# Kernel optimization log

Measured on AMD Instinct MI355X. Metric: run time of the kernel, lower is better.

Reference implementation:

```python
import jax, jax.numpy as jnp
import numpy as np

LAMBDA_GEO = 0.5


def setup_inputs() -> dict:
    key = jax.random.key(0)
    embeddings = jax.random.normal(key, (4, 2048, 512), dtype=jnp.float32)
    return {"embeddings": embeddings}


def _geometric_loss(embeddings):
    b, s, d = embeddings.shape
    x = embeddings.reshape(b * s, d)  # [N, d]
    sq_norm = jnp.sum(x * x, axis=-1)  # [N]
    sq = sq_norm[:, None] + sq_norm[None, :] - 2.0 * (x @ x.T)  # [N, N]
    sq = jnp.maximum(sq, 0.0)
    dist = jnp.sqrt(sq)  # torch.cdist(p=2)
    return jnp.mean(jnp.exp(-dist * 0.1)) * 0.1


def reference(embeddings):
    geometric_loss = _geometric_loss(embeddings)
    total_geometric = LAMBDA_GEO * geometric_loss
    return geometric_loss, total_geometric
```

## Files before the change

kernel.cpp:

```cpp
#include <hip/hip_runtime.h>

#define NROWS 8192
#define DIM   512
#define NT    64
#define NTRI  (NT * (NT + 1) / 2)
#define NACC  64

typedef __attribute__((ext_vector_type(16))) float f32x16;
typedef __attribute__((ext_vector_type(8)))  int   i32x8;

__device__ __forceinline__ unsigned char f2e4m3(float x) {
    unsigned ux = __float_as_uint(x);
    unsigned s  = (ux >> 24) & 0x80u;
    float a = __uint_as_float(ux & 0x7FFFFFFFu);
    a = fminf(a, 448.0f);
    unsigned ua = __float_as_uint(a);
    int eb = (int)(ua >> 23);
    if (eb < 121) eb = 121;
    float step  = __uint_as_float((unsigned)(eb - 3) << 23);
    float istep = __uint_as_float((unsigned)(257 - eb) << 23);
    float q = rintf(a * istep) * step;
    q = fminf(q, 448.0f);
    if (q < 0.001953125f)
        return (unsigned char)s;
    unsigned uq = __float_as_uint(q);
    int eq = (int)(uq >> 23) - 127;
    unsigned byte;
    if (eq < -6) byte = (unsigned)(q * 512.0f);
    else         byte = (unsigned)((eq + 7) << 3) | ((uq >> 20) & 7u);
    return (unsigned char)(s | byte);
}

__global__ __launch_bounds__(256) void norm_convert_kernel(
    const float* __restrict__ X, unsigned char* __restrict__ Xq,
    float* __restrict__ norms, float* __restrict__ acc)
{
    const int tid  = threadIdx.x;
    const int lane = tid & 63;
    const int w    = tid >> 6;
    const int row  = blockIdx.x * 4 + w;

    if (blockIdx.x == 0 && tid < NACC) acc[tid] = 0.0f;

    const float* xr = X + (size_t)row * DIM + lane * 8;
    float4 v0 = *(const float4*)xr;
    float4 v1 = *(const float4*)(xr + 4);

    float s = 0.0f;
    s = fmaf(v0.x, v0.x, s); s = fmaf(v0.y, v0.y, s);
    s = fmaf(v0.z, v0.z, s); s = fmaf(v0.w, v0.w, s);
    s = fmaf(v1.x, v1.x, s); s = fmaf(v1.y, v1.y, s);
    s = fmaf(v1.z, v1.z, s); s = fmaf(v1.w, v1.w, s);

    union { unsigned char b[8]; uint2 v; } pk;
    pk.b[0] = f2e4m3(v0.x); pk.b[1] = f2e4m3(v0.y);
    pk.b[2] = f2e4m3(v0.z); pk.b[3] = f2e4m3(v0.w);
    pk.b[4] = f2e4m3(v1.x); pk.b[5] = f2e4m3(v1.y);
    pk.b[6] = f2e4m3(v1.z); pk.b[7] = f2e4m3(v1.w);

    const int slab = lane >> 3;
    const int cpos = (lane & 7) ^ (row & 7);
    *(uint2*)(Xq + (size_t)row * DIM + slab * 64 + cpos * 8) = pk.v;

    #pragma unroll
    for (int off = 32; off > 0; off >>= 1) s += __shfl_down(s, off, 64);
    if (lane == 0) norms[row] = s;
}

__device__ __forceinline__ void gload16(const void* g, void* l) {
    __builtin_amdgcn_global_load_lds(
        (const __attribute__((address_space(1))) unsigned int*)g,
        (__attribute__((address_space(3))) unsigned int*)l, 16, 0, 0);
}

__global__ __launch_bounds__(256, 4) void pair_loss_gemm_kernel(
    const unsigned char* __restrict__ Xq, const float* __restrict__ norms,
    float* __restrict__ acc)
{
    __shared__ __align__(16) char As0[8192];
    __shared__ __align__(16) char As1[8192];
    __shared__ __align__(16) char Bs0[8192];
    __shared__ __align__(16) char Bs1[8192];
    __shared__ float wsum[4];

    int t = blockIdx.x, bi = 0;
    while (t >= (NT - bi)) { t -= (NT - bi); bi++; }
    const int bj = bi + t;

    const int tid  = threadIdx.x;
    const int lane = tid & 63;
    const int w    = tid >> 6;

    const int rowA = bi * 128;
    const int rowB = bj * 128;

    f32x16 accv[2][2];
    #pragma unroll
    for (int a = 0; a < 2; a++)
        #pragma unroll
        for (int b = 0; b < 2; b++)
            #pragma unroll
            for (int r = 0; r < 16; r++) accv[a][b][r] = 0.0f;

    const int rs = w * 32 + (lane >> 2);
    const int cs = (lane & 3) * 16;
    const unsigned char* sA0 = Xq + (size_t)(rowA + rs) * DIM + cs;
    const unsigned char* sA1 = sA0 + (size_t)16 * DIM;
    const unsigned char* sB0 = Xq + (size_t)(rowB + rs) * DIM + cs;
    const unsigned char* sB1 = sB0 + (size_t)16 * DIM;
    const int ldw = w * 2048;

    const int rl = lane & 31;
    const int qh = lane >> 5;
    const int sw = lane & 7;
    const int wr = (w & 1) * 64;
    const int wc = (w >> 1) * 64;
    const int raoff = (wr + rl) * 64;
    const int rboff = (wc + rl) * 64;

    gload16(sA0, As0 + ldw);
    gload16(sA1, As0 + ldw + 1024);
    gload16(sB0, Bs0 + ldw);
    gload16(sB1, Bs0 + ldw + 1024);
    __syncthreads();

    char* curA = As0; char* nxtA = As1;
    char* curB = Bs0; char* nxtB = Bs1;

    #pragma unroll 1
    for (int k = 0; k < 8; k++) {
        const bool more = (k < 7);
        if (more) {
            const int ko = (k + 1) * 64;
            gload16(sA0 + ko, nxtA + ldw);
            gload16(sA1 + ko, nxtA + ldw + 1024);
            gload16(sB0 + ko, nxtB + ldw);
            gload16(sB1 + ko, nxtB + ldw + 1024);
        }

        union { long l[4]; i32x8 v; } fa0, fa1, fb0, fb1;
        #pragma unroll
        for (int i = 0; i < 4; i++) {
            const int fo = ((4 * qh + i) ^ sw) * 8;
            fa0.l[i] = *(const long*)(curA + raoff + fo);
            fa1.l[i] = *(const long*)(curA + raoff + 2048 + fo);
            fb0.l[i] = *(const long*)(curB + rboff + fo);
            fb1.l[i] = *(const long*)(curB + rboff + 2048 + fo);
        }

        accv[0][0] = __builtin_amdgcn_mfma_scale_f32_32x32x64_f8f6f4(
            fa0.v, fb0.v, accv[0][0], 0, 0, 0, 0x7F7F7F7F, 0, 0x7F7F7F7F);
        accv[0][1] = __builtin_amdgcn_mfma_scale_f32_32x32x64_f8f6f4(
            fa0.v, fb1.v, accv[0][1], 0, 0, 0, 0x7F7F7F7F, 0, 0x7F7F7F7F);
        accv[1][0] = __builtin_amdgcn_mfma_scale_f32_32x32x64_f8f6f4(
            fa1.v, fb0.v, accv[1][0], 0, 0, 0, 0x7F7F7F7F, 0, 0x7F7F7F7F);
        accv[1][1] = __builtin_amdgcn_mfma_scale_f32_32x32x64_f8f6f4(
            fa1.v, fb1.v, accv[1][1], 0, 0, 0, 0x7F7F7F7F, 0, 0x7F7F7F7F);

        if (more) {
            __syncthreads();
            char* tA = curA; curA = nxtA; nxtA = tA;
            char* tB = curB; curB = nxtB; nxtB = tB;
        }
    }

    const float wgt = (bi == bj) ? 1.0f : 2.0f;
    const int cl = lane & 31;
    const int rh = (lane >> 5) * 4;
    float lsum = 0.0f;
    #pragma unroll
    for (int a = 0; a < 2; a++) {
        const int gia = rowA + wr + a * 32;
        float ni[16];
        #pragma unroll
        for (int r = 0; r < 16; r++)
            ni[r] = norms[gia + (r & 3) + 8 * (r >> 2) + rh];
        #pragma unroll
        for (int b = 0; b < 2; b++) {
            const int gj = rowB + wc + b * 32 + cl;
            const float nj = norms[gj];
            #pragma unroll
            for (int r = 0; r < 16; r++) {
                const int gi = gia + (r & 3) + 8 * (r >> 2) + rh;
                float sq = fmaf(-2.0f, accv[a][b][r], ni[r] + nj);
                sq = fmaxf(sq, 0.0f);
                float term = __expf(-0.1f * sqrtf(sq));
                if (gi == gj) term = 1.0f;
                lsum += term;
            }
        }
    }
    lsum *= wgt;
    #pragma unroll
    for (int off = 32; off > 0; off >>= 1) lsum += __shfl_down(lsum, off, 64);
    if (lane == 0) wsum[w] = lsum;
    __syncthreads();
    if (tid == 0)
        atomicAdd(&acc[blockIdx.x & (NACC - 1)],
                  wsum[0] + wsum[1] + wsum[2] + wsum[3]);
}

__global__ void finalize_kernel(const float* __restrict__ acc,
                                float* __restrict__ out)
{
    const int lane = threadIdx.x;
    float s = (lane < NACC) ? acc[lane] : 0.0f;
    #pragma unroll
    for (int off = 32; off > 0; off >>= 1) s += __shfl_down(s, off, 64);
    if (lane == 0) {
        const float inv = 1.0f / ((float)NROWS * (float)NROWS);
        float loss = s * inv * 0.1f;
        out[0] = loss;
        out[1] = 0.5f * loss;
    }
}

extern "C" void kernel_launch(void* const* d_in, const int* in_sizes, int n_in,
                              void* d_out, int out_size, void* d_ws, size_t ws_size,
                              hipStream_t stream)
{
    const float* X = (const float*)d_in[0];
    float* out = (float*)d_out;

    char* ws = (char*)d_ws;
    float*         acc   = (float*)ws;
    float*         norms = (float*)(ws + 1024);
    unsigned char* Xq    = (unsigned char*)(ws + 1024 + 32768);

    norm_convert_kernel<<<NROWS / 4, 256, 0, stream>>>(X, Xq, norms, acc);
    pair_loss_gemm_kernel<<<NTRI, 256, 0, stream>>>(Xq, norms, acc);
    finalize_kernel<<<1, 64, 0, stream>>>(acc, out);
}
```

Before: 106.3 us.

## Double K-step per stage, 16-byte swizzled LDS reads, fuse finalize via last-block counter

The GEMM stage now loads 128 bytes of K per step (two 64-wide slabs), halving loop iterations and barriers. The fp8 swizzle changes from 8-byte to 16-byte granularity so fragments are read with uint4 LDS loads. setprio is raised around the MFMA block. The separate finalize kernel is replaced by a last-block atomic counter that reduces the accumulators in-kernel, saving a launch. LDS doubles to 64KB per block and occupancy hint drops from 4 to 2 blocks per CU.

```diff
diff --git a/kernel.cpp b/kernel.cpp
--- a/kernel.cpp
+++ b/kernel.cpp
@@ -40,7 +40,7 @@
     const int w    = tid >> 6;
     const int row  = blockIdx.x * 4 + w;
 
-    if (blockIdx.x == 0 && tid < NACC) acc[tid] = 0.0f;
+    if (blockIdx.x == 0 && tid < NACC + 1) acc[tid] = 0.0f;
 
     const float* xr = X + (size_t)row * DIM + lane * 8;
     float4 v0 = *(const float4*)xr;
@@ -59,8 +59,10 @@
     pk.b[6] = f2e4m3(v1.z); pk.b[7] = f2e4m3(v1.w);
 
     const int slab = lane >> 3;
-    const int cpos = (lane & 7) ^ (row & 7);
-    *(uint2*)(Xq + (size_t)row * DIM + slab * 64 + cpos * 8) = pk.v;
+    const int c16  = (lane >> 1) & 3;
+    const int cpos = c16 ^ ((row >> 1) & 3);
+    *(uint2*)(Xq + (size_t)row * DIM + slab * 64 + cpos * 16 + (lane & 1) * 8)
+        = pk.v;
 
     #pragma unroll
     for (int off = 32; off > 0; off >>= 1) s += __shfl_down(s, off, 64);
@@ -73,15 +75,16 @@
         (__attribute__((address_space(3))) unsigned int*)l, 16, 0, 0);
 }
 
-__global__ __launch_bounds__(256, 4) void pair_loss_gemm_kernel(
+__global__ __launch_bounds__(256, 2) void pair_loss_gemm_kernel(
     const unsigned char* __restrict__ Xq, const float* __restrict__ norms,
-    float* __restrict__ acc)
+    float* __restrict__ acc, float* __restrict__ out)
 {
-    __shared__ __align__(16) char As0[8192];
-    __shared__ __align__(16) char As1[8192];
-    __shared__ __align__(16) char Bs0[8192];
-    __shared__ __align__(16) char Bs1[8192];
+    __shared__ __align__(16) char As0[16384];
+    __shared__ __align__(16) char As1[16384];
+    __shared__ __align__(16) char Bs0[16384];
+    __shared__ __align__(16) char Bs1[16384];
     __shared__ float wsum[4];
+    __shared__ int lastflag;
 
     int t = blockIdx.x, bi = 0;
     while (t >= (NT - bi)) { t -= (NT - bi); bi++; }
@@ -102,60 +105,72 @@
             #pragma unroll
             for (int r = 0; r < 16; r++) accv[a][b][r] = 0.0f;
 
-    const int rs = w * 32 + (lane >> 2);
-    const int cs = (lane & 3) * 16;
-    const unsigned char* sA0 = Xq + (size_t)(rowA + rs) * DIM + cs;
-    const unsigned char* sA1 = sA0 + (size_t)16 * DIM;
-    const unsigned char* sB0 = Xq + (size_t)(rowB + rs) * DIM + cs;
-    const unsigned char* sB1 = sB0 + (size_t)16 * DIM;
-    const int ldw = w * 2048;
+    const int lrow = lane >> 2;
+    const int lpos = ((lane & 3) ^ ((lane >> 3) & 3)) * 16;
+    const unsigned char* gA =
+        Xq + (size_t)(rowA + w * 32 + lrow) * DIM + lpos;
+    const unsigned char* gB =
+        Xq + (size_t)(rowB + w * 32 + lrow) * DIM + lpos;
+    char* const ldst0 = (char*)0 + (w * 32) * 64;
 
     const int rl = lane & 31;
     const int qh = lane >> 5;
-    const int sw = lane & 7;
+    const int p0 = ((2 * qh) ^ ((rl >> 1) & 3)) * 16;
+    const int p1 = p0 ^ 16;
     const int wr = (w & 1) * 64;
     const int wc = (w >> 1) * 64;
-    const int raoff = (wr + rl) * 64;
-    const int rboff = (wc + rl) * 64;
-
-    gload16(sA0, As0 + ldw);
-    gload16(sA1, As0 + ldw + 1024);
-    gload16(sB0, Bs0 + ldw);
-    gload16(sB1, Bs0 + ldw + 1024);
+    const int ra = (wr + rl) * 64;
+    const int rb = (wc + rl) * 64;
+
+#define STAGE(bufA, bufB, k) do {                                        \
+        const int kb_ = (k) * 128;                                       \
+        gload16(gA + kb_,             (bufA) + (w * 32) * 64);           \
+        gload16(gA + kb_ + 16 * DIM,  (bufA) + (w * 32 + 16) * 64);      \
+        gload16(gA + kb_ + 64,        (bufA) + 8192 + (w * 32) * 64);    \
+        gload16(gA + kb_ + 16 * DIM + 64,                                \
+                (bufA) + 8192 + (w * 32 + 16) * 64);                     \
+        gload16(gB + kb_,             (bufB) + (w * 32) * 64);           \
+        gload16(gB + kb_ + 16 * DIM,  (bufB) + (w * 32 + 16) * 64);      \
+        gload16(gB + kb_ + 64,        (bufB) + 8192 + (w * 32) * 64);    \
+        gload16(gB + kb_ + 16 * DIM + 64,                                \
+                (bufB) + 8192 + (w * 32 + 16) * 64);                     \
+    } while (0)
+
+    STAGE(As0, Bs0, 0);
     __syncthreads();
 
     char* curA = As0; char* nxtA = As1;
     char* curB = Bs0; char* nxtB = Bs1;
 
     #pragma unroll 1
-    for (int k = 0; k < 8; k++) {
-        const bool more = (k < 7);
-        if (more) {
-            const int ko = (k + 1) * 64;
-            gload16(sA0 + ko, nxtA + ldw);
-            gload16(sA1 + ko, nxtA + ldw + 1024);
-            gload16(sB0 + ko, nxtB + ldw);
-            gload16(sB1 + ko, nxtB + ldw + 1024);
-        }
-
-        union { long l[4]; i32x8 v; } fa0, fa1, fb0, fb1;
-        #pragma unroll
-        for (int i = 0; i < 4; i++) {
-            const int fo = ((4 * qh + i) ^ sw) * 8;
-            fa0.l[i] = *(const long*)(curA + raoff + fo);
-            fa1.l[i] = *(const long*)(curA + raoff + 2048 + fo);
-            fb0.l[i] = *(const long*)(curB + rboff + fo);
-            fb1.l[i] = *(const long*)(curB + rboff + 2048 + fo);
-        }
-
-        accv[0][0] = __builtin_amdgcn_mfma_scale_f32_32x32x64_f8f6f4(
-            fa0.v, fb0.v, accv[0][0], 0, 0, 0, 0x7F7F7F7F, 0, 0x7F7F7F7F);
-        accv[0][1] = __builtin_amdgcn_mfma_scale_f32_32x32x64_f8f6f4(
-            fa0.v, fb1.v, accv[0][1], 0, 0, 0, 0x7F7F7F7F, 0, 0x7F7F7F7F);
-        accv[1][0] = __builtin_amdgcn_mfma_scale_f32_32x32x64_f8f6f4(
-            fa1.v, fb0.v, accv[1][0], 0, 0, 0, 0x7F7F7F7F, 0, 0x7F7F7F7F);
-        accv[1][1] = __builtin_amdgcn_mfma_scale_f32_32x32x64_f8f6f4(
-            fa1.v, fb1.v, accv[1][1], 0, 0, 0, 0x7F7F7F7F, 0, 0x7F7F7F7F);
+    for (int k = 0; k < 4; k++) {
+        const bool more = (k < 3);
+        if (more) STAGE(nxtA, nxtB, k + 1);
+
+        __builtin_amdgcn_s_setprio(1);
+        #pragma unroll
+        for (int s = 0; s < 2; s++) {
+            const int sb = s * 8192;
+            union { uint4 u[2]; i32x8 v; } fa0, fa1, fb0, fb1;
+            fa0.u[0] = *(const uint4*)(curA + sb + ra + p0);
+            fa0.u[1] = *(const uint4*)(curA + sb + ra + p1);
+            fa1.u[0] = *(const uint4*)(curA + sb + ra + 2048 + p0);
+            fa1.u[1] = *(const uint4*)(curA + sb + ra + 2048 + p1);
+            fb0.u[0] = *(const uint4*)(curB + sb + rb + p0);
+            fb0.u[1] = *(const uint4*)(curB + sb + rb + p1);
+            fb1.u[0] = *(const uint4*)(curB + sb + rb + 2048 + p0);
+            fb1.u[1] = *(const uint4*)(curB + sb + rb + 2048 + p1);
+
+            accv[0][0] = __builtin_amdgcn_mfma_scale_f32_32x32x64_f8f6f4(
+                fa0.v, fb0.v, accv[0][0], 0, 0, 0, 0x7F7F7F7F, 0, 0x7F7F7F7F);
+            accv[0][1] = __builtin_amdgcn_mfma_scale_f32_32x32x64_f8f6f4(
+                fa0.v, fb1.v, accv[0][1], 0, 0, 0, 0x7F7F7F7F, 0, 0x7F7F7F7F);
+            accv[1][0] = __builtin_amdgcn_mfma_scale_f32_32x32x64_f8f6f4(
+                fa1.v, fb0.v, accv[1][0], 0, 0, 0, 0x7F7F7F7F, 0, 0x7F7F7F7F);
+            accv[1][1] = __builtin_amdgcn_mfma_scale_f32_32x32x64_f8f6f4(
+                fa1.v, fb1.v, accv[1][1], 0, 0, 0, 0x7F7F7F7F, 0, 0x7F7F7F7F);
+        }
+        __builtin_amdgcn_s_setprio(0);
 
         if (more) {
             __syncthreads();
@@ -163,6 +178,7 @@
             char* tB = curB; curB = nxtB; nxtB = tB;
         }
     }
+#undef STAGE
 
     const float wgt = (bi == bj) ? 1.0f : 2.0f;
     const int cl = lane & 31;
@@ -195,23 +211,25 @@
     for (int off = 32; off > 0; off >>= 1) lsum += __shfl_down(lsum, off, 64);
     if (lane == 0) wsum[w] = lsum;
     __syncthreads();
-    if (tid == 0)
-        atomicAdd(&acc[blockIdx.x & (NACC - 1)],
-                  wsum[0] + wsum[1] + wsum[2] + wsum[3]);
-}
-
-__global__ void finalize_kernel(const float* __restrict__ acc,
-                                float* __restrict__ out)
-{
-    const int lane = threadIdx.x;
-    float s = (lane < NACC) ? acc[lane] : 0.0f;
-    #pragma unroll
-    for (int off = 32; off > 0; off >>= 1) s += __shfl_down(s, off, 64);
-    if (lane == 0) {
-        const float inv = 1.0f / ((float)NROWS * (float)NROWS);
-        float loss = s * inv * 0.1f;
-        out[0] = loss;
-        out[1] = 0.5f * loss;
+
+    if (tid == 0) {
+        float bsum = wsum[0] + wsum[1] + wsum[2] + wsum[3];
+        float old = atomicAdd(&acc[blockIdx.x & (NACC - 1)], bsum);
+        asm volatile("" :: "v"(old));
+        unsigned prev = atomicAdd((unsigned int*)(acc + NACC), 1u);
+        lastflag = (prev == NTRI - 1) ? 1 : 0;
+    }
+    __syncthreads();
+    if (lastflag && tid < 64) {
+        float v = atomicAdd(&acc[tid], 0.0f);
+        #pragma unroll
+        for (int off = 32; off > 0; off >>= 1) v += __shfl_down(v, off, 64);
+        if (tid == 0) {
+            const float inv = 1.0f / ((float)NROWS * (float)NROWS);
+            float loss = v * inv * 0.1f;
+            out[0] = loss;
+            out[1] = 0.5f * loss;
+        }
     }
 }
 
@@ -228,6 +246,5 @@
     unsigned char* Xq    = (unsigned char*)(ws + 1024 + 32768);
 
     norm_convert_kernel<<<NROWS / 4, 256, 0, stream>>>(X, Xq, norms, acc);
-    pair_loss_gemm_kernel<<<NTRI, 256, 0, stream>>>(Xq, norms, acc);
-    finalize_kernel<<<1, 64, 0, stream>>>(acc, out);
-}
+    pair_loss_gemm_kernel<<<NTRI, 256, 0, stream>>>(Xq, norms, acc, out);
+}
```

After: 115.8 us. 1.09x slower.
